# Optimization experiments

Measured on AMD Instinct MI355X. Metric: run time of the kernel, lower is better.

Reference implementation:

```python
import jax, jax.numpy as jnp
import numpy as np

PRECISION = 127.0

def _pwb_quantize(t):
    # Pulse-width binary mapping: clip to [-1, 1] (layer constraint) and
    # quantize to `precision` discrete levels, as PWBMapper realizes weights.
    t = jnp.clip(t, -1.0, 1.0)
    return jnp.round(t * PRECISION) / PRECISION

def setup_inputs() -> dict:
    key = jax.random.key(0)
    k1, k2, k3 = jax.random.split(key, 3)
    B, DIN, DOUT = 4096, 2048, 2048
    x = jax.random.normal(k1, (B, DIN), dtype=jnp.float32)
    # tf.random_normal_initializer default stddev = 0.05
    W = jax.random.normal(k2, (DIN, DOUT), dtype=jnp.float32) * 0.05
    b = jax.random.normal(k3, (DOUT,), dtype=jnp.float32) * 0.05
    return {"x": x, "W": W, "b": b}

def reference(x, W, b):
    # Fused equivalent of the per-sample / per-neuron Python loops:
    # each neuron's PWB step is a dot product with the quantized weight
    # column; the bias neuron adds the quantized bias. Then activation.
    Wq = _pwb_quantize(W)            # [DIN, DOUT]
    bq = _pwb_quantize(b)            # [DOUT]
    y = jnp.einsum('bi,io->bo', x, Wq) + bq
    return jax.nn.relu(y)
```

## Files before the change

### kernel.cpp

```cpp
#include <hip/hip_runtime.h>
#include <hip/hip_bf16.h>
#include <stdint.h>


typedef __attribute__((ext_vector_type(4))) int i32x4;

#define BM 128
#define BN 128
#define BK 64

__device__ __forceinline__ float pwb_clip(float w) {
    return fminf(fmaxf(w, -1.f), 1.f);
}

__device__ __forceinline__ void gl16(const int8_t* g, int8_t* l) {
    __builtin_amdgcn_global_load_lds(
        (const __attribute__((address_space(1))) void*)(g),
        (__attribute__((address_space(3))) void*)(l),
        16, 0, 0);
}

#define WAIT_LGKM0 { asm volatile("s_waitcnt lgkmcnt(0)" ::: "memory"); \
                     __builtin_amdgcn_sched_barrier(0); }
#define WAIT_VM4   asm volatile("s_waitcnt vmcnt(4)" ::: "memory");
#define WAIT_VM0   asm volatile("s_waitcnt vmcnt(0)" ::: "memory");
#define BAR()      __builtin_amdgcn_s_barrier();

__global__ void pwb_quant_x(const float* __restrict__ x, int8_t* __restrict__ xq,
                            float* __restrict__ scales, int K) {
    const int row = blockIdx.x * 4 + (threadIdx.x >> 6);
    const int l   = threadIdx.x & 63;
    const float4* xr = (const float4*)(x + (size_t)row * K);
    const int J = K >> 8;
    float m = 0.f;
    for (int j = 0; j < J; ++j) {
        float4 v = xr[j * 64 + l];
        m = fmaxf(m, fmaxf(fmaxf(fabsf(v.x), fabsf(v.y)),
                           fmaxf(fabsf(v.z), fabsf(v.w))));
    }
#pragma unroll
    for (int d = 1; d < 64; d <<= 1) m = fmaxf(m, __shfl_xor(m, d));
    const float r = (m > 0.f) ? 127.f / m : 0.f;
    if (l == 0) scales[row] = m / 16129.f;
    uint32_t* o = (uint32_t*)(xq + (size_t)row * K);
    for (int j = 0; j < J; ++j) {
        float4 v = xr[j * 64 + l];
        int q0 = (int)rintf(v.x * r), q1 = (int)rintf(v.y * r);
        int q2 = (int)rintf(v.z * r), q3 = (int)rintf(v.w * r);
        uint32_t u = (uint32_t)(q0 & 255) | ((uint32_t)(q1 & 255) << 8) |
                     ((uint32_t)(q2 & 255) << 16) | ((uint32_t)(q3 & 255) << 24);
        o[j * 64 + l] = u;
    }
}

__global__ void pwb_quant_w(const float* __restrict__ W, int8_t* __restrict__ Wq,
                            int DIN, int DOUT) {
    __shared__ int8_t t[32][36];
    const int tx = threadIdx.x;
    const int ty = threadIdx.y;
    const int c0 = blockIdx.x * 32;
    const int r0 = blockIdx.y * 32;
#pragma unroll
    for (int i = 0; i < 4; ++i) {
        int row = r0 + ty + i * 8;
        float w = W[(size_t)row * DOUT + c0 + tx];
        t[tx][ty + i * 8] = (int8_t)rintf(pwb_clip(w) * 127.f);
    }
    __syncthreads();
    const int tt = ty * 32 + tx;
    const int lr = tt >> 3, wd = tt & 7;
    uint32_t u = (uint32_t)(uint8_t)t[lr][wd * 4 + 0]
               | ((uint32_t)(uint8_t)t[lr][wd * 4 + 1] << 8)
               | ((uint32_t)(uint8_t)t[lr][wd * 4 + 2] << 16)
               | ((uint32_t)(uint8_t)t[lr][wd * 4 + 3] << 24);
    ((uint32_t*)(Wq + (size_t)(c0 + lr) * DIN + r0))[wd] = u;
}

__global__ __launch_bounds__(256, 2) void pwb_gemmq(
    const int8_t* __restrict__ A,
    const int8_t* __restrict__ Bt,
    const float* __restrict__ scales,
    const float* __restrict__ b,
    float* __restrict__ C,
    int M, int N, int K, int GN, int nwg) {
    __shared__ __align__(16) int8_t lA[3][BM * BK];
    __shared__ __align__(16) int8_t lB[3][BN * BK];

    const int tid = threadIdx.x;
    const int w   = tid >> 6;
    const int l   = tid & 63;
    const int lr  = l & 15;
    const int lk  = l >> 4;

    const int bid = blockIdx.x;
    const int q = nwg >> 3, r = nwg & 7;
    const int xcd = bid & 7, lin = bid >> 3;
    const int wgid = (xcd < r ? xcd * (q + 1) : r * (q + 1) + (xcd - r) * q) + lin;
    const int tm = wgid / GN, tn = wgid % GN;
    const size_t brow = (size_t)tm * BM, bcol = (size_t)tn * BN;

    const int wm = (w >> 1) * 64;
    const int wn = (w & 1) * 64;

    const int s0 = tid, s1 = tid + 256;
    const int r0c = s0 >> 2, k0c = (s0 & 3) ^ ((s0 >> 3) & 3);
    const int r1c = s1 >> 2, k1c = (s1 & 3) ^ ((s1 >> 3) & 3);
    const int8_t* gA0 = A  + (size_t)(brow + r0c) * K + k0c * 16;
    const int8_t* gA1 = A  + (size_t)(brow + r1c) * K + k1c * 16;
    const int8_t* gB0 = Bt + (size_t)(bcol + r0c) * K + k0c * 16;
    const int8_t* gB1 = Bt + (size_t)(bcol + r1c) * K + k1c * 16;

    const int offAb = (wm + lr) * 64 + ((lk ^ ((lr >> 1) & 3)) << 4);
    const int offBb = (wn + lr) * 64 + ((lk ^ ((lr >> 1) & 3)) << 4);

    i32x4 acc[4][4] = {};

    const int T = K / BK;

#define STAGE(buf, ktg)                              \
    gl16(gA0 + (ktg), &lA[buf][w * 1024]);           \
    gl16(gA1 + (ktg), &lA[buf][w * 1024 + 4096]);    \
    gl16(gB0 + (ktg), &lB[buf][w * 1024]);           \
    gl16(gB1 + (ktg), &lB[buf][w * 1024 + 4096]);

#define DS_FRAGS(cA, cB)                                      \
    i32x4 af[4], bfr[4];                                      \
    _Pragma("unroll") for (int mi = 0; mi < 4; ++mi)          \
        af[mi] = *(const i32x4*)&(cA)[offAb + mi * 1024];     \
    _Pragma("unroll") for (int nj = 0; nj < 4; ++nj)          \
        bfr[nj] = *(const i32x4*)&(cB)[offBb + nj * 1024];

#define MFMA16                                                 \
    __builtin_amdgcn_s_setprio(1);                             \
    _Pragma("unroll") for (int mi = 0; mi < 4; ++mi)           \
    _Pragma("unroll") for (int nj = 0; nj < 4; ++nj)           \
        acc[mi][nj] = __builtin_amdgcn_mfma_i32_16x16x64_i8(   \
            af[mi], bfr[nj], acc[mi][nj], 0, 0, 0);            \
    __builtin_amdgcn_s_setprio(0);

    STAGE(0, 0)
    STAGE(1, BK)
    WAIT_VM4
    BAR();

    int cur = 0;
    for (int t = 0; t < T - 2; ++t) {
        int nb = cur + 2; if (nb >= 3) nb -= 3;
        const int8_t* cA = &lA[cur][0];
        const int8_t* cB = &lB[cur][0];
        {
            DS_FRAGS(cA, cB)
            STAGE(nb, (t + 2) * BK)
            BAR();
            WAIT_LGKM0
            MFMA16
        }
        WAIT_VM4
        BAR();
        cur = (cur == 2) ? 0 : cur + 1;
    }
    {
        const int8_t* cA = &lA[cur][0];
        const int8_t* cB = &lB[cur][0];
        DS_FRAGS(cA, cB)
        BAR();
        WAIT_LGKM0
        MFMA16
        WAIT_VM0
        BAR();
        cur = (cur == 2) ? 0 : cur + 1;
    }
    {
        const int8_t* cA = &lA[cur][0];
        const int8_t* cB = &lB[cur][0];
        DS_FRAGS(cA, cB)
        WAIT_LGKM0
        MFMA16
    }

    float bias[4];
#pragma unroll
    for (int nj = 0; nj < 4; ++nj) {
        float bv = b[bcol + wn + nj * 16 + lr];
        bias[nj] = rintf(pwb_clip(bv) * 127.f) * (1.f / 127.f);
    }

    const size_t orow = brow + wm + lk * 4;
    const size_t ocol = bcol + wn + lr;
    float scl[4][4];
#pragma unroll
    for (int mi = 0; mi < 4; ++mi)
#pragma unroll
        for (int rg = 0; rg < 4; ++rg)
            scl[mi][rg] = scales[orow + mi * 16 + rg];

#pragma unroll
    for (int mi = 0; mi < 4; ++mi)
#pragma unroll
        for (int nj = 0; nj < 4; ++nj)
#pragma unroll
            for (int rg = 0; rg < 4; ++rg) {
                float v = fmaf((float)acc[mi][nj][rg], scl[mi][rg], bias[nj]);
                C[(orow + mi * 16 + rg) * N + (ocol + nj * 16)] = fmaxf(v, 0.f);
            }
#undef STAGE
#undef DS_FRAGS
#undef MFMA16
}

__global__ void pwb_fallback(const float* __restrict__ x, const float* __restrict__ W,
                             const float* __restrict__ b, float* __restrict__ out,
                             int M, int N, int K) {
    __shared__ float sA[16][17];
    __shared__ float sB[16][17];
    int tx = threadIdx.x, ty = threadIdx.y;
    int row = blockIdx.y * 16 + ty;
    int col = blockIdx.x * 16 + tx;
    float acc = 0.f;
    for (int kt = 0; kt < K; kt += 16) {
        sA[ty][tx] = (row < M && kt + tx < K) ? x[(size_t)row * K + kt + tx] : 0.f;
        float w = (kt + ty < K && col < N) ? W[(size_t)(kt + ty) * N + col] : 0.f;
        sB[ty][tx] = rintf(pwb_clip(w) * 127.f) * (1.f / 127.f);
        __syncthreads();
#pragma unroll
        for (int kk = 0; kk < 16; ++kk) acc += sA[ty][kk] * sB[kk][tx];
        __syncthreads();
    }
    if (row < M && col < N) {
        float v = acc + rintf(pwb_clip(b[col]) * 127.f) * (1.f / 127.f);
        out[(size_t)row * N + col] = fmaxf(v, 0.f);
    }
}

extern "C" void kernel_launch(void* const* d_in, const int* in_sizes, int n_in,
                              void* d_out, int out_size, void* d_ws, size_t ws_size,
                              hipStream_t stream) {
    const float* x = (const float*)d_in[0];
    const float* W = (const float*)d_in[1];
    const float* b = (const float*)d_in[2];
    float* out = (float*)d_out;

    const int DOUT = in_sizes[2];
    const int DIN  = in_sizes[1] / DOUT;
    const int M    = in_sizes[0] / DIN;

    size_t need = (size_t)M * DIN + (size_t)DIN * DOUT + (size_t)M * 4;
    bool fast = (M % BM == 0) && (M % 4 == 0) && (DOUT % BN == 0) &&
                (DIN % 256 == 0) && (DIN >= 2 * BK) &&
                (DOUT % 32 == 0) && (DIN % 32 == 0) && (ws_size >= need);

    if (fast) {
        int8_t* xq = (int8_t*)d_ws;
        int8_t* Wq = xq + (size_t)M * DIN;
        float* scales = (float*)(Wq + (size_t)DIN * DOUT);

        pwb_quant_x<<<M / 4, 256, 0, stream>>>(x, xq, scales, DIN);
        pwb_quant_w<<<dim3(DOUT / 32, DIN / 32), dim3(32, 8), 0, stream>>>(W, Wq, DIN, DOUT);

        const int GM = M / BM, GN = DOUT / BN, nwg = GM * GN;
        pwb_gemmq<<<nwg, 256, 0, stream>>>(xq, Wq, scales, b, out, M, DOUT, DIN, GN, nwg);
    } else {
        dim3 g((DOUT + 15) / 16, (M + 15) / 16), blk(16, 16);
        pwb_fallback<<<g, blk, 0, stream>>>(x, W, b, out, M, DOUT, DIN);
    }
}
```

Baseline: 42.38 us.

## Enlarge GEMM tile to 256x128, merge quantization kernels, vectorize scale loads

Doubles the M tile of the int8 MFMA GEMM to 256 rows, so each wave computes 128x64 with 32 accumulators and issues six async LDS loads per stage. Launch bounds drop to one block per SIMD occupancy target. The separate x and W quantization kernels are merged into one launch, and row scales are read as float4 in the epilogue. The larger tile is meant to raise operand reuse and cut launch overhead, at the cost of more registers and LDS, lower occupancy, and half as many workgroups (256) across the CUs.

```diff
diff --git a/kernel.cpp b/kernel.cpp
--- a/kernel.cpp
+++ b/kernel.cpp
@@ -5,7 +5,7 @@
 
 typedef __attribute__((ext_vector_type(4))) int i32x4;
 
-#define BM 128
+#define BM 256
 #define BN 128
 #define BK 64
 
@@ -22,61 +22,62 @@
 
 #define WAIT_LGKM0 { asm volatile("s_waitcnt lgkmcnt(0)" ::: "memory"); \
                      __builtin_amdgcn_sched_barrier(0); }
-#define WAIT_VM4   asm volatile("s_waitcnt vmcnt(4)" ::: "memory");
+#define WAIT_VM6   asm volatile("s_waitcnt vmcnt(6)" ::: "memory");
 #define WAIT_VM0   asm volatile("s_waitcnt vmcnt(0)" ::: "memory");
 #define BAR()      __builtin_amdgcn_s_barrier();
 
-__global__ void pwb_quant_x(const float* __restrict__ x, int8_t* __restrict__ xq,
-                            float* __restrict__ scales, int K) {
-    const int row = blockIdx.x * 4 + (threadIdx.x >> 6);
-    const int l   = threadIdx.x & 63;
-    const float4* xr = (const float4*)(x + (size_t)row * K);
-    const int J = K >> 8;
-    float m = 0.f;
-    for (int j = 0; j < J; ++j) {
-        float4 v = xr[j * 64 + l];
-        m = fmaxf(m, fmaxf(fmaxf(fabsf(v.x), fabsf(v.y)),
-                           fmaxf(fabsf(v.z), fabsf(v.w))));
-    }
-#pragma unroll
-    for (int d = 1; d < 64; d <<= 1) m = fmaxf(m, __shfl_xor(m, d));
-    const float r = (m > 0.f) ? 127.f / m : 0.f;
-    if (l == 0) scales[row] = m / 16129.f;
-    uint32_t* o = (uint32_t*)(xq + (size_t)row * K);
-    for (int j = 0; j < J; ++j) {
-        float4 v = xr[j * 64 + l];
-        int q0 = (int)rintf(v.x * r), q1 = (int)rintf(v.y * r);
-        int q2 = (int)rintf(v.z * r), q3 = (int)rintf(v.w * r);
-        uint32_t u = (uint32_t)(q0 & 255) | ((uint32_t)(q1 & 255) << 8) |
-                     ((uint32_t)(q2 & 255) << 16) | ((uint32_t)(q3 & 255) << 24);
-        o[j * 64 + l] = u;
-    }
-}
-
-__global__ void pwb_quant_w(const float* __restrict__ W, int8_t* __restrict__ Wq,
-                            int DIN, int DOUT) {
+__global__ void pwb_prep(const float* __restrict__ x, const float* __restrict__ W,
+                         int8_t* __restrict__ xq, int8_t* __restrict__ Wq,
+                         float* __restrict__ scales, int DIN, int DOUT, int xblocks) {
     __shared__ int8_t t[32][36];
-    const int tx = threadIdx.x;
-    const int ty = threadIdx.y;
-    const int c0 = blockIdx.x * 32;
-    const int r0 = blockIdx.y * 32;
-#pragma unroll
-    for (int i = 0; i < 4; ++i) {
-        int row = r0 + ty + i * 8;
-        float w = W[(size_t)row * DOUT + c0 + tx];
-        t[tx][ty + i * 8] = (int8_t)rintf(pwb_clip(w) * 127.f);
-    }
-    __syncthreads();
-    const int tt = ty * 32 + tx;
-    const int lr = tt >> 3, wd = tt & 7;
-    uint32_t u = (uint32_t)(uint8_t)t[lr][wd * 4 + 0]
-               | ((uint32_t)(uint8_t)t[lr][wd * 4 + 1] << 8)
-               | ((uint32_t)(uint8_t)t[lr][wd * 4 + 2] << 16)
-               | ((uint32_t)(uint8_t)t[lr][wd * 4 + 3] << 24);
-    ((uint32_t*)(Wq + (size_t)(c0 + lr) * DIN + r0))[wd] = u;
-}
-
-__global__ __launch_bounds__(256, 2) void pwb_gemmq(
+    const int tid = threadIdx.x;
+    if ((int)blockIdx.x < xblocks) {
+        const int row = blockIdx.x * 4 + (tid >> 6);
+        const int l   = tid & 63;
+        const float4* xr = (const float4*)(x + (size_t)row * DIN);
+        const int J = DIN >> 8;
+        float m = 0.f;
+        for (int j = 0; j < J; ++j) {
+            float4 v = xr[j * 64 + l];
+            m = fmaxf(m, fmaxf(fmaxf(fabsf(v.x), fabsf(v.y)),
+                               fmaxf(fabsf(v.z), fabsf(v.w))));
+        }
+#pragma unroll
+        for (int d = 1; d < 64; d <<= 1) m = fmaxf(m, __shfl_xor(m, d));
+        const float r = (m > 0.f) ? 127.f / m : 0.f;
+        if (l == 0) scales[row] = m / 16129.f;
+        uint32_t* o = (uint32_t*)(xq + (size_t)row * DIN);
+        for (int j = 0; j < J; ++j) {
+            float4 v = xr[j * 64 + l];
+            int q0 = (int)rintf(v.x * r), q1 = (int)rintf(v.y * r);
+            int q2 = (int)rintf(v.z * r), q3 = (int)rintf(v.w * r);
+            uint32_t u = (uint32_t)(q0 & 255) | ((uint32_t)(q1 & 255) << 8) |
+                         ((uint32_t)(q2 & 255) << 16) | ((uint32_t)(q3 & 255) << 24);
+            o[j * 64 + l] = u;
+        }
+    } else {
+        const int wb = blockIdx.x - xblocks;
+        const int gw = DOUT >> 5;
+        const int c0 = (wb % gw) * 32;
+        const int r0 = (wb / gw) * 32;
+        const int tx = tid & 31, ty = tid >> 5;
+#pragma unroll
+        for (int i = 0; i < 4; ++i) {
+            int row = r0 + ty + i * 8;
+            float w = W[(size_t)row * DOUT + c0 + tx];
+            t[tx][ty + i * 8] = (int8_t)rintf(pwb_clip(w) * 127.f);
+        }
+        __syncthreads();
+        const int lr = tid >> 3, wd = tid & 7;
+        uint32_t u = (uint32_t)(uint8_t)t[lr][wd * 4 + 0]
+                   | ((uint32_t)(uint8_t)t[lr][wd * 4 + 1] << 8)
+                   | ((uint32_t)(uint8_t)t[lr][wd * 4 + 2] << 16)
+                   | ((uint32_t)(uint8_t)t[lr][wd * 4 + 3] << 24);
+        ((uint32_t*)(Wq + (size_t)(c0 + lr) * DIN + r0))[wd] = u;
+    }
+}
+
+__global__ __launch_bounds__(256, 1) void pwb_gemmq(
     const int8_t* __restrict__ A,
     const int8_t* __restrict__ Bt,
     const float* __restrict__ scales,
@@ -99,40 +100,50 @@
     const int tm = wgid / GN, tn = wgid % GN;
     const size_t brow = (size_t)tm * BM, bcol = (size_t)tn * BN;
 
-    const int wm = (w >> 1) * 64;
+    const int wm = (w >> 1) * 128;
     const int wn = (w & 1) * 64;
 
-    const int s0 = tid, s1 = tid + 256;
-    const int r0c = s0 >> 2, k0c = (s0 & 3) ^ ((s0 >> 3) & 3);
-    const int r1c = s1 >> 2, k1c = (s1 & 3) ^ ((s1 >> 3) & 3);
-    const int8_t* gA0 = A  + (size_t)(brow + r0c) * K + k0c * 16;
-    const int8_t* gA1 = A  + (size_t)(brow + r1c) * K + k1c * 16;
-    const int8_t* gB0 = Bt + (size_t)(bcol + r0c) * K + k0c * 16;
-    const int8_t* gB1 = Bt + (size_t)(bcol + r1c) * K + k1c * 16;
-
-    const int offAb = (wm + lr) * 64 + ((lk ^ ((lr >> 1) & 3)) << 4);
-    const int offBb = (wn + lr) * 64 + ((lk ^ ((lr >> 1) & 3)) << 4);
-
-    i32x4 acc[4][4] = {};
+    const int8_t* gAp[4];
+    const int8_t* gBp[2];
+#pragma unroll
+    for (int i = 0; i < 4; ++i) {
+        int s = tid + 256 * i;
+        int rr = s >> 2, kc = (s & 3) ^ ((s >> 3) & 3);
+        gAp[i] = A + (size_t)(brow + rr) * K + kc * 16;
+    }
+#pragma unroll
+    for (int i = 0; i < 2; ++i) {
+        int s = tid + 256 * i;
+        int rr = s >> 2, kc = (s & 3) ^ ((s >> 3) & 3);
+        gBp[i] = Bt + (size_t)(bcol + rr) * K + kc * 16;
+    }
+
+    const int xk    = (lk ^ ((lr >> 1) & 3)) << 4;
+    const int offAb = (wm + lr) * 64 + xk;
+    const int offBb = (wn + lr) * 64 + xk;
+
+    i32x4 acc[8][4] = {};
 
     const int T = K / BK;
 
-#define STAGE(buf, ktg)                              \
-    gl16(gA0 + (ktg), &lA[buf][w * 1024]);           \
-    gl16(gA1 + (ktg), &lA[buf][w * 1024 + 4096]);    \
-    gl16(gB0 + (ktg), &lB[buf][w * 1024]);           \
-    gl16(gB1 + (ktg), &lB[buf][w * 1024 + 4096]);
+#define STAGE(buf, ktg)                                \
+    gl16(gAp[0] + (ktg), &lA[buf][w * 1024]);          \
+    gl16(gAp[1] + (ktg), &lA[buf][w * 1024 + 4096]);   \
+    gl16(gAp[2] + (ktg), &lA[buf][w * 1024 + 8192]);   \
+    gl16(gAp[3] + (ktg), &lA[buf][w * 1024 + 12288]);  \
+    gl16(gBp[0] + (ktg), &lB[buf][w * 1024]);          \
+    gl16(gBp[1] + (ktg), &lB[buf][w * 1024 + 4096]);
 
 #define DS_FRAGS(cA, cB)                                      \
-    i32x4 af[4], bfr[4];                                      \
-    _Pragma("unroll") for (int mi = 0; mi < 4; ++mi)          \
+    i32x4 af[8], bfr[4];                                      \
+    _Pragma("unroll") for (int mi = 0; mi < 8; ++mi)          \
         af[mi] = *(const i32x4*)&(cA)[offAb + mi * 1024];     \
     _Pragma("unroll") for (int nj = 0; nj < 4; ++nj)          \
         bfr[nj] = *(const i32x4*)&(cB)[offBb + nj * 1024];
 
-#define MFMA16                                                 \
+#define MFMA32                                                 \
     __builtin_amdgcn_s_setprio(1);                             \
-    _Pragma("unroll") for (int mi = 0; mi < 4; ++mi)           \
+    _Pragma("unroll") for (int mi = 0; mi < 8; ++mi)           \
     _Pragma("unroll") for (int nj = 0; nj < 4; ++nj)           \
         acc[mi][nj] = __builtin_amdgcn_mfma_i32_16x16x64_i8(   \
             af[mi], bfr[nj], acc[mi][nj], 0, 0, 0);            \
@@ -140,7 +151,7 @@
 
     STAGE(0, 0)
     STAGE(1, BK)
-    WAIT_VM4
+    WAIT_VM6
     BAR();
 
     int cur = 0;
@@ -153,9 +164,9 @@
             STAGE(nb, (t + 2) * BK)
             BAR();
             WAIT_LGKM0
-            MFMA16
-        }
-        WAIT_VM4
+            MFMA32
+        }
+        WAIT_VM6
         BAR();
         cur = (cur == 2) ? 0 : cur + 1;
     }
@@ -165,7 +176,7 @@
         DS_FRAGS(cA, cB)
         BAR();
         WAIT_LGKM0
-        MFMA16
+        MFMA32
         WAIT_VM0
         BAR();
         cur = (cur == 2) ? 0 : cur + 1;
@@ -175,7 +186,7 @@
         const int8_t* cB = &lB[cur][0];
         DS_FRAGS(cA, cB)
         WAIT_LGKM0
-        MFMA16
+        MFMA32
     }
 
     float bias[4];
@@ -187,25 +198,30 @@
 
     const size_t orow = brow + wm + lk * 4;
     const size_t ocol = bcol + wn + lr;
-    float scl[4][4];
-#pragma unroll
-    for (int mi = 0; mi < 4; ++mi)
-#pragma unroll
-        for (int rg = 0; rg < 4; ++rg)
-            scl[mi][rg] = scales[orow + mi * 16 + rg];
-
-#pragma unroll
-    for (int mi = 0; mi < 4; ++mi)
-#pragma unroll
-        for (int nj = 0; nj < 4; ++nj)
-#pragma unroll
-            for (int rg = 0; rg < 4; ++rg) {
-                float v = fmaf((float)acc[mi][nj][rg], scl[mi][rg], bias[nj]);
-                C[(orow + mi * 16 + rg) * N + (ocol + nj * 16)] = fmaxf(v, 0.f);
-            }
+    float4 scl[8];
+#pragma unroll
+    for (int mi = 0; mi < 8; ++mi)
+        scl[mi] = *(const float4*)&scales[orow + mi * 16];
+
+#pragma unroll
+    for (int mi = 0; mi < 8; ++mi) {
+        const float s0 = scl[mi].x, s1 = scl[mi].y, s2 = scl[mi].z, s3 = scl[mi].w;
+#pragma unroll
+        for (int nj = 0; nj < 4; ++nj) {
+            float v0 = fmaf((float)acc[mi][nj][0], s0, bias[nj]);
+            float v1 = fmaf((float)acc[mi][nj][1], s1, bias[nj]);
+            float v2 = fmaf((float)acc[mi][nj][2], s2, bias[nj]);
+            float v3 = fmaf((float)acc[mi][nj][3], s3, bias[nj]);
+            float* cp = &C[(orow + mi * 16) * N + (ocol + nj * 16)];
+            cp[0 * N] = fmaxf(v0, 0.f);
+            cp[1 * N] = fmaxf(v1, 0.f);
+            cp[2 * N] = fmaxf(v2, 0.f);
+            cp[3 * N] = fmaxf(v3, 0.f);
+        }
+    }
 #undef STAGE
 #undef DS_FRAGS
-#undef MFMA16
+#undef MFMA32
 }
 
 __global__ void pwb_fallback(const float* __restrict__ x, const float* __restrict__ W,
@@ -245,7 +261,7 @@
     const int M    = in_sizes[0] / DIN;
 
     size_t need = (size_t)M * DIN + (size_t)DIN * DOUT + (size_t)M * 4;
-    bool fast = (M % BM == 0) && (M % 4 == 0) && (DOUT % BN == 0) &&
+    bool fast = (M % BM == 0) && (DOUT % BN == 0) &&
                 (DIN % 256 == 0) && (DIN >= 2 * BK) &&
                 (DOUT % 32 == 0) && (DIN % 32 == 0) && (ws_size >= need);
 
@@ -254,8 +270,10 @@
         int8_t* Wq = xq + (size_t)M * DIN;
         float* scales = (float*)(Wq + (size_t)DIN * DOUT);
 
-        pwb_quant_x<<<M / 4, 256, 0, stream>>>(x, xq, scales, DIN);
-        pwb_quant_w<<<dim3(DOUT / 32, DIN / 32), dim3(32, 8), 0, stream>>>(W, Wq, DIN, DOUT);
+        const int xblocks = M / 4;
+        const int wblocks = (DOUT / 32) * (DIN / 32);
+        pwb_prep<<<xblocks + wblocks, 256, 0, stream>>>(x, W, xq, Wq, scales,
+                                                        DIN, DOUT, xblocks);
 
         const int GM = M / BM, GN = DOUT / BN, nwg = GM * GN;
         pwb_gemmq<<<nwg, 256, 0, stream>>>(xq, Wq, scales, b, out, M, DOUT, DIN, GN, nwg);
```

After: 45.81 us. 8.1% more time.

## Merge quantization kernels and register-double-buffer fragments in 4-stage int8 GEMM pipeline

Applied to the files above, without the earlier changes.

Fuses the x and W quantization kernels into a single launch with block-index dispatch, removing one kernel launch. The GEMM moves from a 3-buffer LDS ring with an explicit lgkmcnt wait before the MFMAs to a 4-buffer ring with ping-pong register fragments. Fragments for the next tile are read from LDS while the MFMAs for the current tile issue, hiding LDS latency. The epilogue loads scales as float4. LDS use rises to 64KB per block, which may limit occupancy, and the fast path now requires an even number of K tiles.

```diff
diff --git a/kernel.cpp b/kernel.cpp
--- a/kernel.cpp
+++ b/kernel.cpp
@@ -20,60 +20,59 @@
         16, 0, 0);
 }
 
-#define WAIT_LGKM0 { asm volatile("s_waitcnt lgkmcnt(0)" ::: "memory"); \
-                     __builtin_amdgcn_sched_barrier(0); }
 #define WAIT_VM4   asm volatile("s_waitcnt vmcnt(4)" ::: "memory");
 #define WAIT_VM0   asm volatile("s_waitcnt vmcnt(0)" ::: "memory");
 #define BAR()      __builtin_amdgcn_s_barrier();
 
-__global__ void pwb_quant_x(const float* __restrict__ x, int8_t* __restrict__ xq,
-                            float* __restrict__ scales, int K) {
-    const int row = blockIdx.x * 4 + (threadIdx.x >> 6);
-    const int l   = threadIdx.x & 63;
-    const float4* xr = (const float4*)(x + (size_t)row * K);
-    const int J = K >> 8;
-    float m = 0.f;
-    for (int j = 0; j < J; ++j) {
-        float4 v = xr[j * 64 + l];
-        m = fmaxf(m, fmaxf(fmaxf(fabsf(v.x), fabsf(v.y)),
-                           fmaxf(fabsf(v.z), fabsf(v.w))));
-    }
-#pragma unroll
-    for (int d = 1; d < 64; d <<= 1) m = fmaxf(m, __shfl_xor(m, d));
-    const float r = (m > 0.f) ? 127.f / m : 0.f;
-    if (l == 0) scales[row] = m / 16129.f;
-    uint32_t* o = (uint32_t*)(xq + (size_t)row * K);
-    for (int j = 0; j < J; ++j) {
-        float4 v = xr[j * 64 + l];
-        int q0 = (int)rintf(v.x * r), q1 = (int)rintf(v.y * r);
-        int q2 = (int)rintf(v.z * r), q3 = (int)rintf(v.w * r);
-        uint32_t u = (uint32_t)(q0 & 255) | ((uint32_t)(q1 & 255) << 8) |
-                     ((uint32_t)(q2 & 255) << 16) | ((uint32_t)(q3 & 255) << 24);
-        o[j * 64 + l] = u;
-    }
-}
-
-__global__ void pwb_quant_w(const float* __restrict__ W, int8_t* __restrict__ Wq,
-                            int DIN, int DOUT) {
+__global__ void pwb_prep(const float* __restrict__ x, const float* __restrict__ W,
+                         int8_t* __restrict__ xq, int8_t* __restrict__ Wq,
+                         float* __restrict__ scales, int DIN, int DOUT, int xblocks) {
     __shared__ int8_t t[32][36];
-    const int tx = threadIdx.x;
-    const int ty = threadIdx.y;
-    const int c0 = blockIdx.x * 32;
-    const int r0 = blockIdx.y * 32;
-#pragma unroll
-    for (int i = 0; i < 4; ++i) {
-        int row = r0 + ty + i * 8;
-        float w = W[(size_t)row * DOUT + c0 + tx];
-        t[tx][ty + i * 8] = (int8_t)rintf(pwb_clip(w) * 127.f);
-    }
-    __syncthreads();
-    const int tt = ty * 32 + tx;
-    const int lr = tt >> 3, wd = tt & 7;
-    uint32_t u = (uint32_t)(uint8_t)t[lr][wd * 4 + 0]
-               | ((uint32_t)(uint8_t)t[lr][wd * 4 + 1] << 8)
-               | ((uint32_t)(uint8_t)t[lr][wd * 4 + 2] << 16)
-               | ((uint32_t)(uint8_t)t[lr][wd * 4 + 3] << 24);
-    ((uint32_t*)(Wq + (size_t)(c0 + lr) * DIN + r0))[wd] = u;
+    const int tid = threadIdx.x;
+    if ((int)blockIdx.x < xblocks) {
+        const int row = blockIdx.x * 4 + (tid >> 6);
+        const int l   = tid & 63;
+        const float4* xr = (const float4*)(x + (size_t)row * DIN);
+        const int J = DIN >> 8;
+        float m = 0.f;
+        for (int j = 0; j < J; ++j) {
+            float4 v = xr[j * 64 + l];
+            m = fmaxf(m, fmaxf(fmaxf(fabsf(v.x), fabsf(v.y)),
+                               fmaxf(fabsf(v.z), fabsf(v.w))));
+        }
+#pragma unroll
+        for (int d = 1; d < 64; d <<= 1) m = fmaxf(m, __shfl_xor(m, d));
+        const float r = (m > 0.f) ? 127.f / m : 0.f;
+        if (l == 0) scales[row] = m / 16129.f;
+        uint32_t* o = (uint32_t*)(xq + (size_t)row * DIN);
+        for (int j = 0; j < J; ++j) {
+            float4 v = xr[j * 64 + l];
+            int q0 = (int)rintf(v.x * r), q1 = (int)rintf(v.y * r);
+            int q2 = (int)rintf(v.z * r), q3 = (int)rintf(v.w * r);
+            uint32_t u = (uint32_t)(q0 & 255) | ((uint32_t)(q1 & 255) << 8) |
+                         ((uint32_t)(q2 & 255) << 16) | ((uint32_t)(q3 & 255) << 24);
+            o[j * 64 + l] = u;
+        }
+    } else {
+        const int wb = blockIdx.x - xblocks;
+        const int gw = DOUT >> 5;
+        const int c0 = (wb % gw) * 32;
+        const int r0 = (wb / gw) * 32;
+        const int tx = tid & 31, ty = tid >> 5;
+#pragma unroll
+        for (int i = 0; i < 4; ++i) {
+            int row = r0 + ty + i * 8;
+            float w = W[(size_t)row * DOUT + c0 + tx];
+            t[tx][ty + i * 8] = (int8_t)rintf(pwb_clip(w) * 127.f);
+        }
+        __syncthreads();
+        const int lr = tid >> 3, wd = tid & 7;
+        uint32_t u = (uint32_t)(uint8_t)t[lr][wd * 4 + 0]
+                   | ((uint32_t)(uint8_t)t[lr][wd * 4 + 1] << 8)
+                   | ((uint32_t)(uint8_t)t[lr][wd * 4 + 2] << 16)
+                   | ((uint32_t)(uint8_t)t[lr][wd * 4 + 3] << 24);
+        ((uint32_t*)(Wq + (size_t)(c0 + lr) * DIN + r0))[wd] = u;
+    }
 }
 
 __global__ __launch_bounds__(256, 2) void pwb_gemmq(
@@ -83,8 +82,8 @@
     const float* __restrict__ b,
     float* __restrict__ C,
     int M, int N, int K, int GN, int nwg) {
-    __shared__ __align__(16) int8_t lA[3][BM * BK];
-    __shared__ __align__(16) int8_t lB[3][BN * BK];
+    __shared__ __align__(16) int8_t lA[4][BM * BK];
+    __shared__ __align__(16) int8_t lB[4][BN * BK];
 
     const int tid = threadIdx.x;
     const int w   = tid >> 6;
@@ -110,8 +109,9 @@
     const int8_t* gB0 = Bt + (size_t)(bcol + r0c) * K + k0c * 16;
     const int8_t* gB1 = Bt + (size_t)(bcol + r1c) * K + k1c * 16;
 
-    const int offAb = (wm + lr) * 64 + ((lk ^ ((lr >> 1) & 3)) << 4);
-    const int offBb = (wn + lr) * 64 + ((lk ^ ((lr >> 1) & 3)) << 4);
+    const int xk    = (lk ^ ((lr >> 1) & 3)) << 4;
+    const int offAb = (wm + lr) * 64 + xk;
+    const int offBb = (wn + lr) * 64 + xk;
 
     i32x4 acc[4][4] = {};
 
@@ -123,19 +123,18 @@
     gl16(gB0 + (ktg), &lB[buf][w * 1024]);           \
     gl16(gB1 + (ktg), &lB[buf][w * 1024 + 4096]);
 
-#define DS_FRAGS(cA, cB)                                      \
-    i32x4 af[4], bfr[4];                                      \
-    _Pragma("unroll") for (int mi = 0; mi < 4; ++mi)          \
-        af[mi] = *(const i32x4*)&(cA)[offAb + mi * 1024];     \
-    _Pragma("unroll") for (int nj = 0; nj < 4; ++nj)          \
-        bfr[nj] = *(const i32x4*)&(cB)[offBb + nj * 1024];
-
-#define MFMA16                                                 \
+#define LOADFRAGS(fa, fb, bi)                                  \
+    _Pragma("unroll") for (int mi = 0; mi < 4; ++mi)           \
+        fa[mi] = *(const i32x4*)&lA[bi][offAb + mi * 1024];    \
+    _Pragma("unroll") for (int nj = 0; nj < 4; ++nj)           \
+        fb[nj] = *(const i32x4*)&lB[bi][offBb + nj * 1024];
+
+#define MFMA16(fa, fb)                                         \
     __builtin_amdgcn_s_setprio(1);                             \
     _Pragma("unroll") for (int mi = 0; mi < 4; ++mi)           \
     _Pragma("unroll") for (int nj = 0; nj < 4; ++nj)           \
         acc[mi][nj] = __builtin_amdgcn_mfma_i32_16x16x64_i8(   \
-            af[mi], bfr[nj], acc[mi][nj], 0, 0, 0);            \
+            fa[mi], fb[nj], acc[mi][nj], 0, 0, 0);             \
     __builtin_amdgcn_s_setprio(0);
 
     STAGE(0, 0)
@@ -143,40 +142,33 @@
     WAIT_VM4
     BAR();
 
-    int cur = 0;
-    for (int t = 0; t < T - 2; ++t) {
-        int nb = cur + 2; if (nb >= 3) nb -= 3;
-        const int8_t* cA = &lA[cur][0];
-        const int8_t* cB = &lB[cur][0];
-        {
-            DS_FRAGS(cA, cB)
-            STAGE(nb, (t + 2) * BK)
-            BAR();
-            WAIT_LGKM0
-            MFMA16
-        }
+    i32x4 aA[4], bA[4], aB[4], bB[4];
+    LOADFRAGS(aA, bA, 0)
+
+    int bR = 1, bS = 2;
+    int ktg = 2 * BK;
+    const int halfIters = (T - 2) >> 1;
+    for (int it = 0; it < halfIters; ++it) {
+        STAGE(bS, ktg)
+        ktg += BK;
         WAIT_VM4
         BAR();
-        cur = (cur == 2) ? 0 : cur + 1;
-    }
-    {
-        const int8_t* cA = &lA[cur][0];
-        const int8_t* cB = &lB[cur][0];
-        DS_FRAGS(cA, cB)
+        LOADFRAGS(aB, bB, bR)
+        MFMA16(aA, bA)
+        bR = (bR + 1) & 3; bS = (bS + 1) & 3;
+        STAGE(bS, ktg)
+        ktg += BK;
+        WAIT_VM4
         BAR();
-        WAIT_LGKM0
-        MFMA16
-        WAIT_VM0
-        BAR();
-        cur = (cur == 2) ? 0 : cur + 1;
-    }
-    {
-        const int8_t* cA = &lA[cur][0];
-        const int8_t* cB = &lB[cur][0];
-        DS_FRAGS(cA, cB)
-        WAIT_LGKM0
-        MFMA16
-    }
+        LOADFRAGS(aA, bA, bR)
+        MFMA16(aB, bB)
+        bR = (bR + 1) & 3; bS = (bS + 1) & 3;
+    }
+    WAIT_VM0
+    BAR();
+    LOADFRAGS(aB, bB, bR)
+    MFMA16(aA, bA)
+    MFMA16(aB, bB)
 
     float bias[4];
 #pragma unroll
@@ -187,24 +179,29 @@
 
     const size_t orow = brow + wm + lk * 4;
     const size_t ocol = bcol + wn + lr;
-    float scl[4][4];
+    float4 scl[4];
 #pragma unroll
     for (int mi = 0; mi < 4; ++mi)
-#pragma unroll
-        for (int rg = 0; rg < 4; ++rg)
-            scl[mi][rg] = scales[orow + mi * 16 + rg];
-
-#pragma unroll
-    for (int mi = 0; mi < 4; ++mi)
-#pragma unroll
-        for (int nj = 0; nj < 4; ++nj)
-#pragma unroll
-            for (int rg = 0; rg < 4; ++rg) {
-                float v = fmaf((float)acc[mi][nj][rg], scl[mi][rg], bias[nj]);
-                C[(orow + mi * 16 + rg) * N + (ocol + nj * 16)] = fmaxf(v, 0.f);
-            }
+        scl[mi] = *(const float4*)&scales[orow + mi * 16];
+
+#pragma unroll
+    for (int mi = 0; mi < 4; ++mi) {
+        const float s0_ = scl[mi].x, s1_ = scl[mi].y, s2_ = scl[mi].z, s3_ = scl[mi].w;
+#pragma unroll
+        for (int nj = 0; nj < 4; ++nj) {
+            float v0 = fmaf((float)acc[mi][nj][0], s0_, bias[nj]);
+            float v1 = fmaf((float)acc[mi][nj][1], s1_, bias[nj]);
+            float v2 = fmaf((float)acc[mi][nj][2], s2_, bias[nj]);
+            float v3 = fmaf((float)acc[mi][nj][3], s3_, bias[nj]);
+            float* cp = &C[(orow + mi * 16) * N + (ocol + nj * 16)];
+            cp[0 * N] = fmaxf(v0, 0.f);
+            cp[1 * N] = fmaxf(v1, 0.f);
+            cp[2 * N] = fmaxf(v2, 0.f);
+            cp[3 * N] = fmaxf(v3, 0.f);
+        }
+    }
 #undef STAGE
-#undef DS_FRAGS
+#undef LOADFRAGS
 #undef MFMA16
 }
 
@@ -245,8 +242,9 @@
     const int M    = in_sizes[0] / DIN;
 
     size_t need = (size_t)M * DIN + (size_t)DIN * DOUT + (size_t)M * 4;
+    const int T = DIN / BK;
     bool fast = (M % BM == 0) && (M % 4 == 0) && (DOUT % BN == 0) &&
-                (DIN % 256 == 0) && (DIN >= 2 * BK) &&
+                (DIN % 256 == 0) && (T >= 4) && ((T & 1) == 0) &&
                 (DOUT % 32 == 0) && (DIN % 32 == 0) && (ws_size >= need);
 
     if (fast) {
@@ -254,8 +252,10 @@
         int8_t* Wq = xq + (size_t)M * DIN;
         float* scales = (float*)(Wq + (size_t)DIN * DOUT);
 
-        pwb_quant_x<<<M / 4, 256, 0, stream>>>(x, xq, scales, DIN);
-        pwb_quant_w<<<dim3(DOUT / 32, DIN / 32), dim3(32, 8), 0, stream>>>(W, Wq, DIN, DOUT);
+        const int xblocks = M / 4;
+        const int wblocks = (DOUT / 32) * (DIN / 32);
+        pwb_prep<<<xblocks + wblocks, 256, 0, stream>>>(x, W, xq, Wq, scales,
+                                                        DIN, DOUT, xblocks);
 
         const int GM = M / BM, GN = DOUT / BN, nwg = GM * GN;
         pwb_gemmq<<<nwg, 256, 0, stream>>>(xq, Wq, scales, b, out, M, DOUT, DIN, GN, nwg);
```

Measured after the change: 43.24 us. 2.0% more time.
